# Optimization experiments

Measured on AMD Instinct MI355X. Metric: run time of the kernel, lower is better.

The kernel has to match this reference:

```python
import jax, jax.numpy as jnp
import numpy as np

N_NODES = 100000
N_EDGES = 3200000
N_GRAPHS = 64


def gcn_conv(x, W, b, src, dst, n_nodes):
    # PyG GCNConv: add self-loops, symmetric degree normalization, then
    # out[dst] += norm * (x @ W)[src], plus bias.
    h = x @ W  # [N, out]
    loop = jnp.arange(n_nodes)
    s = jnp.concatenate([src, loop])
    d = jnp.concatenate([dst, loop])
    deg = jax.ops.segment_sum(jnp.ones_like(d, dtype=h.dtype), d, num_segments=n_nodes)
    dinv = jnp.where(deg > 0, jax.lax.rsqrt(deg), 0.0)
    norm = dinv[s] * dinv[d]  # [E+N]
    msg = norm[:, None] * h[s]  # gather + scale
    out = jax.ops.segment_sum(msg, d, num_segments=n_nodes)  # scatter-add
    return out + b


def global_mean_pool(x, batch, num_graphs):
    sums = jax.ops.segment_sum(x, batch, num_segments=num_graphs)
    cnts = jax.ops.segment_sum(jnp.ones((x.shape[0],), x.dtype), batch, num_segments=num_graphs)
    return sums / jnp.maximum(cnts, 1.0)[:, None]


def setup_inputs() -> dict:
    key = jax.random.key(0)
    ks = jax.random.split(key, 12)
    x = jax.random.normal(ks[0], (N_NODES, 128), dtype=jnp.float32)
    edge_index = jax.random.randint(ks[1], (2, N_EDGES), 0, N_NODES, dtype=jnp.int64 if jax.config.jax_enable_x64 else jnp.int32)
    batch = jnp.sort(jax.random.randint(ks[2], (N_NODES,), 0, N_GRAPHS))
    def lin(k, fan_in, fan_out):
        bound = 1.0 / np.sqrt(fan_in)
        kw, kb = jax.random.split(k)
        W = jax.random.uniform(kw, (fan_in, fan_out), minval=-bound, maxval=bound, dtype=jnp.float32)
        b = jax.random.uniform(kb, (fan_out,), minval=-bound, maxval=bound, dtype=jnp.float32)
        return W, b
    W1, b1 = lin(ks[3], 128, 16)
    W2, b2 = lin(ks[4], 16, 32)
    Wf1, bf1 = lin(ks[5], 32, 64)
    Wf2, bf2 = lin(ks[6], 64, 8)
    return {"x": x, "edge_index": edge_index, "batch": batch,
            "W1": W1, "b1": b1, "W2": W2, "b2": b2,
            "Wf1": Wf1, "bf1": bf1, "Wf2": Wf2, "bf2": bf2}


def reference(x, edge_index, batch, W1, b1, W2, b2, Wf1, bf1, Wf2, bf2):
    src, dst = edge_index[0], edge_index[1]
    n = x.shape[0]
    h = jax.nn.relu(gcn_conv(x, W1, b1, src, dst, n))
    h = jax.nn.relu(gcn_conv(h, W2, b2, src, dst, n))
    g = global_mean_pool(h, batch, N_GRAPHS)  # [G, 32]
    g = jax.nn.relu(g @ Wf1 + bf1)
    return g @ Wf2 + bf2  # [G, num_actions]
```

## Files before the change

kernel.cpp:

```cpp
#include <hip/hip_runtime.h>
#include <hip/hip_fp16.h>

#define N_NODES  100000
#define N_EDGES  3200000
#define N_GRAPHS 64

#define BSHIFT   7
#define NBUCK    782
#define CAP      4608
#define PB_BLK   1024
#define PB_CHUNK 3125

#define SCALE1   2097152.0f
#define ISCALE1  (1.0f / 2097152.0f)
#define SCALE2   1048576.0f
#define ISCALE2  (1.0f / 1048576.0f)
#define SCALEP   65536.0f
#define ISCALEP  (1.0f / 65536.0f)


#define EDGEACC(p_, r_, SC) { \
    int d_ = (int)((p_) >> 17); \
    float2 f01_ = __half22float2(*(const __half2*)&(r_).x); \
    float2 f23_ = __half22float2(*(const __half2*)&(r_).y); \
    int* a_ = &acc[d_ * 17 + f4 * 4]; \
    atomicAdd(a_ + 0, __float2int_rn(f01_.x * (SC))); \
    atomicAdd(a_ + 1, __float2int_rn(f01_.y * (SC))); \
    atomicAdd(a_ + 2, __float2int_rn(f23_.x * (SC))); \
    atomicAdd(a_ + 3, __float2int_rn(f23_.y * (SC))); }

__global__ void __launch_bounds__(256) hist_pass(const int* __restrict__ dst,
                                                 unsigned int* __restrict__ histG) {
    __shared__ int hist[NBUCK];
    int t = threadIdx.x;
    int e0 = blockIdx.x * PB_CHUNK;
    for (int i = t; i < NBUCK; i += 256) hist[i] = 0;
    __syncthreads();
    int i = t;
    for (; i + 768 < PB_CHUNK; i += 1024) {
        int a0 = dst[e0 + i];
        int a1 = dst[e0 + i + 256];
        int a2 = dst[e0 + i + 512];
        int a3 = dst[e0 + i + 768];
        atomicAdd(&hist[a0 >> BSHIFT], 1);
        atomicAdd(&hist[a1 >> BSHIFT], 1);
        atomicAdd(&hist[a2 >> BSHIFT], 1);
        atomicAdd(&hist[a3 >> BSHIFT], 1);
    }
    for (; i < PB_CHUNK; i += 256)
        atomicAdd(&hist[dst[e0 + i] >> BSHIFT], 1);
    __syncthreads();
    for (int i2 = t; i2 < NBUCK; i2 += 256)
        histG[blockIdx.x * NBUCK + i2] = (unsigned int)hist[i2];
}

__global__ void __launch_bounds__(256) scan_pass(const unsigned int* __restrict__ histG,
                                                 unsigned int* __restrict__ baseG,
                                                 int* __restrict__ cntG) {
    __shared__ unsigned int s[256];
    int b = blockIdx.x, t = threadIdx.x;
    unsigned int v0 = histG[(t * 4 + 0) * NBUCK + b];
    unsigned int v1 = histG[(t * 4 + 1) * NBUCK + b];
    unsigned int v2 = histG[(t * 4 + 2) * NBUCK + b];
    unsigned int v3 = histG[(t * 4 + 3) * NBUCK + b];
    unsigned int tot = v0 + v1 + v2 + v3;
    s[t] = tot;
    __syncthreads();
    for (int o = 1; o < 256; o <<= 1) {
        unsigned int x = (t >= o) ? s[t - o] : 0;
        __syncthreads();
        s[t] += x;
        __syncthreads();
    }
    unsigned int ex = s[t] - tot;
    unsigned int base = (unsigned int)b * CAP + ex;
    baseG[b * PB_BLK + t * 4 + 0] = base;
    baseG[b * PB_BLK + t * 4 + 1] = base + v0;
    baseG[b * PB_BLK + t * 4 + 2] = base + v0 + v1;
    baseG[b * PB_BLK + t * 4 + 3] = base + v0 + v1 + v2;
    if (t == 255) cntG[b] = (int)(ex + tot);
}

#define PLACE1(d_, s_) { \
    int bb_ = (d_) >> BSHIFT; \
    unsigned int pk_ = ((unsigned int)((d_) & 127) << 17) | (unsigned int)(s_); \
    int slot_ = atomicAdd(&cur[bb_], 1); \
    st[slot_] = pk_; bkt[slot_] = (unsigned short)bb_; }

__global__ void __launch_bounds__(256) place_pass(const int* __restrict__ src,
                                                  const int* __restrict__ dst,
                                                  const unsigned int* __restrict__ histG,
                                                  const unsigned int* __restrict__ baseG,
                                                  unsigned int* __restrict__ stage) {
    __shared__ int off[NBUCK];
    __shared__ int cur[NBUCK];
    __shared__ unsigned int gbase[NBUCK];
    __shared__ int part[256];
    __shared__ unsigned int st[PB_CHUNK];
    __shared__ unsigned short bkt[PB_CHUNK];
    int t = threadIdx.x, blk = blockIdx.x;
    int e0 = blk * PB_CHUNK;

    int b4 = t * 4;
    int h0 = (b4 + 0 < NBUCK) ? (int)histG[blk * NBUCK + b4 + 0] : 0;
    int h1 = (b4 + 1 < NBUCK) ? (int)histG[blk * NBUCK + b4 + 1] : 0;
    int h2 = (b4 + 2 < NBUCK) ? (int)histG[blk * NBUCK + b4 + 2] : 0;
    int h3 = (b4 + 3 < NBUCK) ? (int)histG[blk * NBUCK + b4 + 3] : 0;
    int tot = h0 + h1 + h2 + h3;
    part[t] = tot;
    __syncthreads();
    for (int o = 1; o < 256; o <<= 1) {
        int v = (t >= o) ? part[t - o] : 0;
        __syncthreads();
        part[t] += v;
        __syncthreads();
    }
    int ex = part[t] - tot;
    if (b4 + 0 < NBUCK) { off[b4 + 0] = ex;                cur[b4 + 0] = ex; }
    if (b4 + 1 < NBUCK) { off[b4 + 1] = ex + h0;           cur[b4 + 1] = ex + h0; }
    if (b4 + 2 < NBUCK) { off[b4 + 2] = ex + h0 + h1;      cur[b4 + 2] = ex + h0 + h1; }
    if (b4 + 3 < NBUCK) { off[b4 + 3] = ex + h0 + h1 + h2; cur[b4 + 3] = ex + h0 + h1 + h2; }
    for (int i = t; i < NBUCK; i += 256) gbase[i] = baseG[i * PB_BLK + blk];
    __syncthreads();

    int i = t;
    for (; i + 768 < PB_CHUNK; i += 1024) {
        int d0 = dst[e0 + i],        s0 = src[e0 + i];
        int d1_ = dst[e0 + i + 256], s1_ = src[e0 + i + 256];
        int d2_ = dst[e0 + i + 512], s2_ = src[e0 + i + 512];
        int d3_ = dst[e0 + i + 768], s3_ = src[e0 + i + 768];
        PLACE1(d0, s0); PLACE1(d1_, s1_); PLACE1(d2_, s2_); PLACE1(d3_, s3_);
    }
    for (; i < PB_CHUNK; i += 256) {
        int d = dst[e0 + i], sv = src[e0 + i];
        PLACE1(d, sv);
    }
    __syncthreads();

    for (int i2 = t; i2 < PB_CHUNK; i2 += 256) {
        int b = bkt[i2];
        unsigned int gs = gbase[b] + (unsigned int)(i2 - off[b]);
        if (gs < (unsigned int)(b + 1) * CAP) stage[gs] = st[i2];
    }
}

__global__ void __launch_bounds__(256) bucket_dinv(const unsigned int* __restrict__ stage,
                                                   const int* __restrict__ cntG,
                                                   float* __restrict__ dinv) {
    __shared__ int ldeg[128];
    int b = blockIdx.x, t = threadIdx.x;
    int base = b * CAP;
    int cnt = cntG[b]; if (cnt > CAP) cnt = CAP;
    if (t < 128) ldeg[t] = 0;
    __syncthreads();
    int i0 = t * 4;
    for (; i0 + 4 <= cnt; i0 += 1024) {
        uint4 p = *(const uint4*)(stage + base + i0);
        atomicAdd(&ldeg[p.x >> 17], 1);
        atomicAdd(&ldeg[p.y >> 17], 1);
        atomicAdd(&ldeg[p.z >> 17], 1);
        atomicAdd(&ldeg[p.w >> 17], 1);
    }
    for (int j = i0; j < cnt && j < i0 + 4; j++)
        atomicAdd(&ldeg[stage[base + j] >> 17], 1);
    __syncthreads();
    int v = b * 128 + t;
    if (t < 128 && v < N_NODES) dinv[v] = rsqrtf((float)(ldeg[t] + 1));
}

#define MM1_ROWS 64
__global__ void __launch_bounds__(256) mm1(const float* __restrict__ x,
                                           const float* __restrict__ W,
                                           const float* __restrict__ dinv,
                                           __half* __restrict__ hs) {
    __shared__ float ws[128 * 16];
    __shared__ float xs[MM1_ROWS * 132];
    int t = threadIdx.x;
    int row0 = blockIdx.x * MM1_ROWS;
    for (int i = t; i < 2048; i += 256) ws[i] = W[i];
    for (int i = t; i < 2048; i += 256) {
        int r = i >> 5, c4 = (i & 31) * 4;
        int v = row0 + r;
        float4 val = (v < N_NODES) ? *(const float4*)(x + (size_t)v * 128 + c4)
                                   : make_float4(0.f, 0.f, 0.f, 0.f);
        *(float4*)&xs[r * 132 + c4] = val;
    }
    __syncthreads();
    int row = t >> 2, c4 = (t & 3) * 4;
    int v = row0 + row;
    if (v < N_NODES) {
        float dv = dinv[v];
        float a0 = 0.f, a1 = 0.f, a2 = 0.f, a3 = 0.f;
#pragma unroll
        for (int k = 0; k < 128; k++) {
            float xv = xs[row * 132 + k];
            float4 w4 = *(const float4*)&ws[k * 16 + c4];
            a0 += xv * w4.x; a1 += xv * w4.y; a2 += xv * w4.z; a3 += xv * w4.w;
        }
        __half2 h01 = __floats2half2_rn(a0 * dv, a1 * dv);
        __half2 h23 = __floats2half2_rn(a2 * dv, a3 * dv);
        uint2 o = make_uint2(*(unsigned*)&h01, *(unsigned*)&h23);
        *(uint2*)(hs + (size_t)v * 16 + c4) = o;
    }
}

__global__ void __launch_bounds__(256) gather1(const unsigned int* __restrict__ stage,
                                               const int* __restrict__ cntG,
                                               const __half* __restrict__ hs,
                                               const float* __restrict__ dinv,
                                               const float* __restrict__ b1,
                                               __half* __restrict__ d1) {
    __shared__ int acc[128 * 17];
    int b = blockIdx.x, t = threadIdx.x;
    int base = b * CAP;
    int cnt = cntG[b]; if (cnt > CAP) cnt = CAP;
    for (int i = t; i < 128 * 17; i += 256) acc[i] = 0;
    __syncthreads();
    int f4 = t & 3;
    int q = t >> 2;
    int i0 = q * 16;
    for (; i0 + 16 <= cnt; i0 += 1024) {
        const uint4* sp = (const uint4*)(stage + base + i0);
        uint4 pa = sp[0], pb = sp[1], pc = sp[2], pd = sp[3];
        uint2 r0  = *(const uint2*)(hs + (pa.x & 0x1FFFF) * 16 + f4 * 4);
        uint2 r1  = *(const uint2*)(hs + (pa.y & 0x1FFFF) * 16 + f4 * 4);
        uint2 r2  = *(const uint2*)(hs + (pa.z & 0x1FFFF) * 16 + f4 * 4);
        uint2 r3  = *(const uint2*)(hs + (pa.w & 0x1FFFF) * 16 + f4 * 4);
        uint2 r4  = *(const uint2*)(hs + (pb.x & 0x1FFFF) * 16 + f4 * 4);
        uint2 r5  = *(const uint2*)(hs + (pb.y & 0x1FFFF) * 16 + f4 * 4);
        uint2 r6  = *(const uint2*)(hs + (pb.z & 0x1FFFF) * 16 + f4 * 4);
        uint2 r7  = *(const uint2*)(hs + (pb.w & 0x1FFFF) * 16 + f4 * 4);
        uint2 r8  = *(const uint2*)(hs + (pc.x & 0x1FFFF) * 16 + f4 * 4);
        uint2 r9  = *(const uint2*)(hs + (pc.y & 0x1FFFF) * 16 + f4 * 4);
        uint2 r10 = *(const uint2*)(hs + (pc.z & 0x1FFFF) * 16 + f4 * 4);
        uint2 r11 = *(const uint2*)(hs + (pc.w & 0x1FFFF) * 16 + f4 * 4);
        uint2 r12 = *(const uint2*)(hs + (pd.x & 0x1FFFF) * 16 + f4 * 4);
        uint2 r13 = *(const uint2*)(hs + (pd.y & 0x1FFFF) * 16 + f4 * 4);
        uint2 r14 = *(const uint2*)(hs + (pd.z & 0x1FFFF) * 16 + f4 * 4);
        uint2 r15 = *(const uint2*)(hs + (pd.w & 0x1FFFF) * 16 + f4 * 4);
        EDGEACC(pa.x, r0,  SCALE1); EDGEACC(pa.y, r1,  SCALE1);
        EDGEACC(pa.z, r2,  SCALE1); EDGEACC(pa.w, r3,  SCALE1);
        EDGEACC(pb.x, r4,  SCALE1); EDGEACC(pb.y, r5,  SCALE1);
        EDGEACC(pb.z, r6,  SCALE1); EDGEACC(pb.w, r7,  SCALE1);
        EDGEACC(pc.x, r8,  SCALE1); EDGEACC(pc.y, r9,  SCALE1);
        EDGEACC(pc.z, r10, SCALE1); EDGEACC(pc.w, r11, SCALE1);
        EDGEACC(pd.x, r12, SCALE1); EDGEACC(pd.y, r13, SCALE1);
        EDGEACC(pd.z, r14, SCALE1); EDGEACC(pd.w, r15, SCALE1);
    }
    for (int j = i0; j < cnt && j < i0 + 16; j++) {
        unsigned int p = stage[base + j];
        uint2 r = *(const uint2*)(hs + (p & 0x1FFFF) * 16 + f4 * 4);
        EDGEACC(p, r, SCALE1);
    }
    __syncthreads();
    for (int i = t; i < 2048; i += 256) {
        int n = i >> 4, k = i & 15, v = b * 128 + n;
        if (v < N_NODES) {
            float dv = dinv[v];
            float sum = (float)acc[n * 17 + k] * ISCALE1;
            float self = __half2float(hs[v * 16 + k]);
            float r = dv * (sum + self) + b1[k];
            d1[v * 16 + k] = __float2half(r > 0.f ? dv * r : 0.f);
        }
    }
}

__global__ void __launch_bounds__(256) gather2(const unsigned int* __restrict__ stage,
                                               const int* __restrict__ cntG,
                                               const __half* __restrict__ d1,
                                               const float* __restrict__ dinv,
                                               const float* __restrict__ W2,
                                               const float* __restrict__ b2,
                                               const int* __restrict__ batch,
                                               float* __restrict__ gsum,
                                               float* __restrict__ gcnt) {
    __shared__ int acc[128 * 17];
    __shared__ float wl[512];
    __shared__ int lsum[N_GRAPHS * 32];
    __shared__ int lcnt[N_GRAPHS];
    __shared__ int lbat[128];
    float* accf = (float*)acc;
    int b = blockIdx.x, t = threadIdx.x;
    int base = b * CAP;
    int cnt = cntG[b]; if (cnt > CAP) cnt = CAP;
    for (int i = t; i < 128 * 17; i += 256) acc[i] = 0;
    for (int i = t; i < 512; i += 256) wl[i] = W2[i];
    for (int i = t; i < N_GRAPHS * 32; i += 256) lsum[i] = 0;
    if (t < N_GRAPHS) lcnt[t] = 0;
    if (t < 128) {
        int v = b * 128 + t;
        lbat[t] = (v < N_NODES) ? batch[v] : 0;
    }
    __syncthreads();
    int f4 = t & 3;
    int q = t >> 2;
    int i0 = q * 16;
    for (; i0 + 16 <= cnt; i0 += 1024) {
        const uint4* sp = (const uint4*)(stage + base + i0);
        uint4 pa = sp[0], pb = sp[1], pc = sp[2], pd = sp[3];
        uint2 r0  = *(const uint2*)(d1 + (pa.x & 0x1FFFF) * 16 + f4 * 4);
        uint2 r1  = *(const uint2*)(d1 + (pa.y & 0x1FFFF) * 16 + f4 * 4);
        uint2 r2  = *(const uint2*)(d1 + (pa.z & 0x1FFFF) * 16 + f4 * 4);
        uint2 r3  = *(const uint2*)(d1 + (pa.w & 0x1FFFF) * 16 + f4 * 4);
        uint2 r4  = *(const uint2*)(d1 + (pb.x & 0x1FFFF) * 16 + f4 * 4);
        uint2 r5  = *(const uint2*)(d1 + (pb.y & 0x1FFFF) * 16 + f4 * 4);
        uint2 r6  = *(const uint2*)(d1 + (pb.z & 0x1FFFF) * 16 + f4 * 4);
        uint2 r7  = *(const uint2*)(d1 + (pb.w & 0x1FFFF) * 16 + f4 * 4);
        uint2 r8  = *(const uint2*)(d1 + (pc.x & 0x1FFFF) * 16 + f4 * 4);
        uint2 r9  = *(const uint2*)(d1 + (pc.y & 0x1FFFF) * 16 + f4 * 4);
        uint2 r10 = *(const uint2*)(d1 + (pc.z & 0x1FFFF) * 16 + f4 * 4);
        uint2 r11 = *(const uint2*)(d1 + (pc.w & 0x1FFFF) * 16 + f4 * 4);
        uint2 r12 = *(const uint2*)(d1 + (pd.x & 0x1FFFF) * 16 + f4 * 4);
        uint2 r13 = *(const uint2*)(d1 + (pd.y & 0x1FFFF) * 16 + f4 * 4);
        uint2 r14 = *(const uint2*)(d1 + (pd.z & 0x1FFFF) * 16 + f4 * 4);
        uint2 r15 = *(const uint2*)(d1 + (pd.w & 0x1FFFF) * 16 + f4 * 4);
        EDGEACC(pa.x, r0,  SCALE2); EDGEACC(pa.y, r1,  SCALE2);
        EDGEACC(pa.z, r2,  SCALE2); EDGEACC(pa.w, r3,  SCALE2);
        EDGEACC(pb.x, r4,  SCALE2); EDGEACC(pb.y, r5,  SCALE2);
        EDGEACC(pb.z, r6,  SCALE2); EDGEACC(pb.w, r7,  SCALE2);
        EDGEACC(pc.x, r8,  SCALE2); EDGEACC(pc.y, r9,  SCALE2);
        EDGEACC(pc.z, r10, SCALE2); EDGEACC(pc.w, r11, SCALE2);
        EDGEACC(pd.x, r12, SCALE2); EDGEACC(pd.y, r13, SCALE2);
        EDGEACC(pd.z, r14, SCALE2); EDGEACC(pd.w, r15, SCALE2);
    }
    for (int j = i0; j < cnt && j < i0 + 16; j++) {
        unsigned int p = stage[base + j];
        uint2 r = *(const uint2*)(d1 + (p & 0x1FFFF) * 16 + f4 * 4);
        EDGEACC(p, r, SCALE2);
    }
    __syncthreads();
    for (int i = t; i < 2048; i += 256) {
        int n = i >> 4, k = i & 15, v = b * 128 + n;
        float sum = (float)acc[n * 17 + k] * ISCALE2;
        if (v < N_NODES) sum += __half2float(d1[v * 16 + k]);
        accf[n * 17 + k] = sum;
    }
    __syncthreads();
    int k = t & 31, l0 = t >> 5;
    for (int g = 0; g < 16; g++) {
        int n = l0 + g * 8, v = b * 128 + n;
        if (v < N_NODES) {
            const float* ar = &accf[n * 17];
            float a = 0.f;
#pragma unroll
            for (int j = 0; j < 16; j++) a += ar[j] * wl[j * 32 + k];
            float r = dinv[v] * a + b2[k];
            r = r > 0.f ? r : 0.f;
            int gg = lbat[n];
            atomicAdd(&lsum[gg * 32 + k], __float2int_rn(r * SCALEP));
            if (k == 0) atomicAdd(&lcnt[gg], 1);
        }
    }
    __syncthreads();
    int last = 127; if (b * 128 + last > N_NODES - 1) last = N_NODES - 1 - b * 128;
    int gmin = lbat[0], gmax = lbat[last];
    int ng = gmax - gmin + 1;
    for (int i = t; i < ng * 32; i += 256) {
        int gg = gmin + (i >> 5);
        int iv = lsum[gg * 32 + (i & 31)];
        if (iv != 0) atomicAdd(&gsum[gg * 32 + (i & 31)], (float)iv * ISCALEP);
    }
    for (int i = t; i < ng; i += 256) {
        int iv = lcnt[gmin + i];
        if (iv != 0) atomicAdd(&gcnt[gmin + i], (float)iv);
    }
}

__global__ void head(const float* __restrict__ gsum, const float* __restrict__ gcnt,
                     const float* __restrict__ Wf1, const float* __restrict__ bf1,
                     const float* __restrict__ Wf2, const float* __restrict__ bf2,
                     float* __restrict__ out) {
    __shared__ float gm[64 * 32];
    __shared__ float f1[64 * 64];
    int t = threadIdx.x;
    for (int i = t; i < 2048; i += 1024) {
        int g = i >> 5;
        float c = gcnt[g]; if (c < 1.f) c = 1.f;
        gm[i] = gsum[i] / c;
    }
    __syncthreads();
    for (int i = t; i < 4096; i += 1024) {
        int r = i >> 6, c = i & 63;
        float a = bf1[c];
#pragma unroll
        for (int j = 0; j < 32; j++) a += gm[r * 32 + j] * Wf1[j * 64 + c];
        f1[i] = a > 0.f ? a : 0.f;
    }
    __syncthreads();
    if (t < 512) {
        int r = t >> 3, c = t & 7;
        float a = bf2[c];
#pragma unroll
        for (int j = 0; j < 64; j++) a += f1[r * 64 + j] * Wf2[j * 8 + c];
        out[t] = a;
    }
}

extern "C" void kernel_launch(void* const* d_in, const int* in_sizes, int n_in,
                              void* d_out, int out_size, void* d_ws, size_t ws_size,
                              hipStream_t stream) {
    const float* x   = (const float*)d_in[0];
    const int*   ei  = (const int*)d_in[1];
    const int*   bat = (const int*)d_in[2];
    const float* W1  = (const float*)d_in[3];
    const float* b1  = (const float*)d_in[4];
    const float* W2  = (const float*)d_in[5];
    const float* b2  = (const float*)d_in[6];
    const float* Wf1 = (const float*)d_in[7];
    const float* bf1 = (const float*)d_in[8];
    const float* Wf2 = (const float*)d_in[9];
    const float* bf2 = (const float*)d_in[10];
    const int* src = ei;
    const int* dst = ei + N_EDGES;
    float* out = (float*)d_out;

    char* ws = (char*)d_ws;
    unsigned int* histG = (unsigned int*)(ws + 0);
    unsigned int* baseG = (unsigned int*)(ws + 3202048);
    int*          cntG  = (int*)         (ws + 6404096);
    unsigned int* stage = (unsigned int*)(ws + 6408192);
    float*        dinv  = (float*)       (ws + 20822016);
    float*        gsum  = (float*)       (ws + 21222016);
    float*        gcnt  = (float*)       (ws + 21230208);
    __half*       hs1   = (__half*)      (ws + 21230464);
    __half*       d1    = (__half*)      (ws + 24430464);

    hipMemsetAsync(gsum, 0, (N_GRAPHS * 32 + N_GRAPHS) * sizeof(float), stream);

    hist_pass<<<PB_BLK, 256, 0, stream>>>(dst, histG);
    scan_pass<<<NBUCK, 256, 0, stream>>>(histG, baseG, cntG);
    place_pass<<<PB_BLK, 256, 0, stream>>>(src, dst, histG, baseG, stage);
    bucket_dinv<<<NBUCK, 256, 0, stream>>>(stage, cntG, dinv);

    mm1<<<(N_NODES + MM1_ROWS - 1) / MM1_ROWS, 256, 0, stream>>>(x, W1, dinv, hs1);
    gather1<<<NBUCK, 256, 0, stream>>>(stage, cntG, hs1, dinv, b1, d1);

    gather2<<<NBUCK, 256, 0, stream>>>(stage, cntG, d1, dinv, W2, b2, bat, gsum, gcnt);

    head<<<1, 1024, 0, stream>>>(gsum, gcnt, Wf1, bf1, Wf2, bf2, out);
}
```

Baseline: 233.4 us.

## Compute degrees with global atomics in hist pass, drop bucket_dinv, widen gather blocks

Node degrees are now counted with global atomics inside the histogram pass, and the reciprocal square root is taken in mm1, which also writes dinv. This removes the separate bucket_dinv kernel and its second read of the staged edges. The gather kernels move to 512 threads per block to put more threads on each bucket's edge list. The trade-off is 3.2M global atomics on a 400KB degree array plus a larger memset to zero it.

```diff
diff --git a/kernel.cpp b/kernel.cpp
--- a/kernel.cpp
+++ b/kernel.cpp
@@ -30,7 +30,8 @@
     atomicAdd(a_ + 3, __float2int_rn(f23_.y * (SC))); }
 
 __global__ void __launch_bounds__(256) hist_pass(const int* __restrict__ dst,
-                                                 unsigned int* __restrict__ histG) {
+                                                 unsigned int* __restrict__ histG,
+                                                 int* __restrict__ degG) {
     __shared__ int hist[NBUCK];
     int t = threadIdx.x;
     int e0 = blockIdx.x * PB_CHUNK;
@@ -46,9 +47,16 @@
         atomicAdd(&hist[a1 >> BSHIFT], 1);
         atomicAdd(&hist[a2 >> BSHIFT], 1);
         atomicAdd(&hist[a3 >> BSHIFT], 1);
-    }
-    for (; i < PB_CHUNK; i += 256)
-        atomicAdd(&hist[dst[e0 + i] >> BSHIFT], 1);
+        atomicAdd(&degG[a0], 1);
+        atomicAdd(&degG[a1], 1);
+        atomicAdd(&degG[a2], 1);
+        atomicAdd(&degG[a3], 1);
+    }
+    for (; i < PB_CHUNK; i += 256) {
+        int a = dst[e0 + i];
+        atomicAdd(&hist[a >> BSHIFT], 1);
+        atomicAdd(&degG[a], 1);
+    }
     __syncthreads();
     for (int i2 = t; i2 < NBUCK; i2 += 256)
         histG[blockIdx.x * NBUCK + i2] = (unsigned int)hist[i2];
@@ -144,34 +152,11 @@
     }
 }
 
-__global__ void __launch_bounds__(256) bucket_dinv(const unsigned int* __restrict__ stage,
-                                                   const int* __restrict__ cntG,
-                                                   float* __restrict__ dinv) {
-    __shared__ int ldeg[128];
-    int b = blockIdx.x, t = threadIdx.x;
-    int base = b * CAP;
-    int cnt = cntG[b]; if (cnt > CAP) cnt = CAP;
-    if (t < 128) ldeg[t] = 0;
-    __syncthreads();
-    int i0 = t * 4;
-    for (; i0 + 4 <= cnt; i0 += 1024) {
-        uint4 p = *(const uint4*)(stage + base + i0);
-        atomicAdd(&ldeg[p.x >> 17], 1);
-        atomicAdd(&ldeg[p.y >> 17], 1);
-        atomicAdd(&ldeg[p.z >> 17], 1);
-        atomicAdd(&ldeg[p.w >> 17], 1);
-    }
-    for (int j = i0; j < cnt && j < i0 + 4; j++)
-        atomicAdd(&ldeg[stage[base + j] >> 17], 1);
-    __syncthreads();
-    int v = b * 128 + t;
-    if (t < 128 && v < N_NODES) dinv[v] = rsqrtf((float)(ldeg[t] + 1));
-}
-
 #define MM1_ROWS 64
 __global__ void __launch_bounds__(256) mm1(const float* __restrict__ x,
                                            const float* __restrict__ W,
-                                           const float* __restrict__ dinv,
+                                           const int* __restrict__ degG,
+                                           float* __restrict__ dinv,
                                            __half* __restrict__ hs) {
     __shared__ float ws[128 * 16];
     __shared__ float xs[MM1_ROWS * 132];
@@ -189,7 +174,8 @@
     int row = t >> 2, c4 = (t & 3) * 4;
     int v = row0 + row;
     if (v < N_NODES) {
-        float dv = dinv[v];
+        float dv = rsqrtf((float)(degG[v] + 1));
+        if (c4 == 0) dinv[v] = dv;
         float a0 = 0.f, a1 = 0.f, a2 = 0.f, a3 = 0.f;
 #pragma unroll
         for (int k = 0; k < 128; k++) {
@@ -204,7 +190,7 @@
     }
 }
 
-__global__ void __launch_bounds__(256) gather1(const unsigned int* __restrict__ stage,
+__global__ void __launch_bounds__(512) gather1(const unsigned int* __restrict__ stage,
                                                const int* __restrict__ cntG,
                                                const __half* __restrict__ hs,
                                                const float* __restrict__ dinv,
@@ -214,12 +200,12 @@
     int b = blockIdx.x, t = threadIdx.x;
     int base = b * CAP;
     int cnt = cntG[b]; if (cnt > CAP) cnt = CAP;
-    for (int i = t; i < 128 * 17; i += 256) acc[i] = 0;
+    for (int i = t; i < 128 * 17; i += 512) acc[i] = 0;
     __syncthreads();
     int f4 = t & 3;
     int q = t >> 2;
     int i0 = q * 16;
-    for (; i0 + 16 <= cnt; i0 += 1024) {
+    for (; i0 + 16 <= cnt; i0 += 2048) {
         const uint4* sp = (const uint4*)(stage + base + i0);
         uint4 pa = sp[0], pb = sp[1], pc = sp[2], pd = sp[3];
         uint2 r0  = *(const uint2*)(hs + (pa.x & 0x1FFFF) * 16 + f4 * 4);
@@ -253,7 +239,7 @@
         EDGEACC(p, r, SCALE1);
     }
     __syncthreads();
-    for (int i = t; i < 2048; i += 256) {
+    for (int i = t; i < 2048; i += 512) {
         int n = i >> 4, k = i & 15, v = b * 128 + n;
         if (v < N_NODES) {
             float dv = dinv[v];
@@ -265,7 +251,7 @@
     }
 }
 
-__global__ void __launch_bounds__(256) gather2(const unsigned int* __restrict__ stage,
+__global__ void __launch_bounds__(512) gather2(const unsigned int* __restrict__ stage,
                                                const int* __restrict__ cntG,
                                                const __half* __restrict__ d1,
                                                const float* __restrict__ dinv,
@@ -283,9 +269,9 @@
     int b = blockIdx.x, t = threadIdx.x;
     int base = b * CAP;
     int cnt = cntG[b]; if (cnt > CAP) cnt = CAP;
-    for (int i = t; i < 128 * 17; i += 256) acc[i] = 0;
-    for (int i = t; i < 512; i += 256) wl[i] = W2[i];
-    for (int i = t; i < N_GRAPHS * 32; i += 256) lsum[i] = 0;
+    for (int i = t; i < 128 * 17; i += 512) acc[i] = 0;
+    if (t < 512) wl[t] = W2[t];
+    for (int i = t; i < N_GRAPHS * 32; i += 512) lsum[i] = 0;
     if (t < N_GRAPHS) lcnt[t] = 0;
     if (t < 128) {
         int v = b * 128 + t;
@@ -295,7 +281,7 @@
     int f4 = t & 3;
     int q = t >> 2;
     int i0 = q * 16;
-    for (; i0 + 16 <= cnt; i0 += 1024) {
+    for (; i0 + 16 <= cnt; i0 += 2048) {
         const uint4* sp = (const uint4*)(stage + base + i0);
         uint4 pa = sp[0], pb = sp[1], pc = sp[2], pd = sp[3];
         uint2 r0  = *(const uint2*)(d1 + (pa.x & 0x1FFFF) * 16 + f4 * 4);
@@ -329,7 +315,7 @@
         EDGEACC(p, r, SCALE2);
     }
     __syncthreads();
-    for (int i = t; i < 2048; i += 256) {
+    for (int i = t; i < 2048; i += 512) {
         int n = i >> 4, k = i & 15, v = b * 128 + n;
         float sum = (float)acc[n * 17 + k] * ISCALE2;
         if (v < N_NODES) sum += __half2float(d1[v * 16 + k]);
@@ -337,8 +323,8 @@
     }
     __syncthreads();
     int k = t & 31, l0 = t >> 5;
-    for (int g = 0; g < 16; g++) {
-        int n = l0 + g * 8, v = b * 128 + n;
+    for (int g = 0; g < 8; g++) {
+        int n = l0 + g * 16, v = b * 128 + n;
         if (v < N_NODES) {
             const float* ar = &accf[n * 17];
             float a = 0.f;
@@ -355,12 +341,12 @@
     int last = 127; if (b * 128 + last > N_NODES - 1) last = N_NODES - 1 - b * 128;
     int gmin = lbat[0], gmax = lbat[last];
     int ng = gmax - gmin + 1;
-    for (int i = t; i < ng * 32; i += 256) {
+    for (int i = t; i < ng * 32; i += 512) {
         int gg = gmin + (i >> 5);
         int iv = lsum[gg * 32 + (i & 31)];
         if (iv != 0) atomicAdd(&gsum[gg * 32 + (i & 31)], (float)iv * ISCALEP);
     }
-    for (int i = t; i < ng; i += 256) {
+    for (int i = t; i < ng; i += 512) {
         int iv = lcnt[gmin + i];
         if (iv != 0) atomicAdd(&gcnt[gmin + i], (float)iv);
     }
@@ -416,26 +402,26 @@
 
     char* ws = (char*)d_ws;
     unsigned int* histG = (unsigned int*)(ws + 0);
-    unsigned int* baseG = (unsigned int*)(ws + 3202048);
-    int*          cntG  = (int*)         (ws + 6404096);
-    unsigned int* stage = (unsigned int*)(ws + 6408192);
-    float*        dinv  = (float*)       (ws + 20822016);
-    float*        gsum  = (float*)       (ws + 21222016);
-    float*        gcnt  = (float*)       (ws + 21230208);
-    __half*       hs1   = (__half*)      (ws + 21230464);
-    __half*       d1    = (__half*)      (ws + 24430464);
-
-    hipMemsetAsync(gsum, 0, (N_GRAPHS * 32 + N_GRAPHS) * sizeof(float), stream);
-
-    hist_pass<<<PB_BLK, 256, 0, stream>>>(dst, histG);
+    unsigned int* baseG = (unsigned int*)(ws + 3203072);
+    int*          cntG  = (int*)         (ws + 6406144);
+    unsigned int* stage = (unsigned int*)(ws + 6410240);
+    float*        dinv  = (float*)       (ws + 20824064);
+    float*        gsum  = (float*)       (ws + 21224064);
+    float*        gcnt  = (float*)       (ws + 21232256);
+    int*          degG  = (int*)         (ws + 21232512);
+    __half*       hs1   = (__half*)      (ws + 21632512);
+    __half*       d1    = (__half*)      (ws + 24832512);
+
+    hipMemsetAsync(gsum, 0, 408448, stream);
+
+    hist_pass<<<PB_BLK, 256, 0, stream>>>(dst, histG, degG);
     scan_pass<<<NBUCK, 256, 0, stream>>>(histG, baseG, cntG);
     place_pass<<<PB_BLK, 256, 0, stream>>>(src, dst, histG, baseG, stage);
-    bucket_dinv<<<NBUCK, 256, 0, stream>>>(stage, cntG, dinv);
-
-    mm1<<<(N_NODES + MM1_ROWS - 1) / MM1_ROWS, 256, 0, stream>>>(x, W1, dinv, hs1);
-    gather1<<<NBUCK, 256, 0, stream>>>(stage, cntG, hs1, dinv, b1, d1);
-
-    gather2<<<NBUCK, 256, 0, stream>>>(stage, cntG, d1, dinv, W2, b2, bat, gsum, gcnt);
+
+    mm1<<<(N_NODES + MM1_ROWS - 1) / MM1_ROWS, 256, 0, stream>>>(x, W1, degG, dinv, hs1);
+    gather1<<<NBUCK, 512, 0, stream>>>(stage, cntG, hs1, dinv, b1, d1);
+
+    gather2<<<NBUCK, 512, 0, stream>>>(stage, cntG, d1, dinv, W2, b2, bat, gsum, gcnt);
 
     head<<<1, 1024, 0, stream>>>(gsum, gcnt, Wf1, bf1, Wf2, bf2, out);
 }
```

After: 358.5 us. 1.54x slower.
